# Optimization experiments

Measured on AMD Instinct MI355X. Metric: run time of the kernel, lower is better.

## Reference

```python
import jax, jax.numpy as jnp
from jax import lax
import numpy as np

B, S, G = 64, 200, 8
CHAR_V, GAZ_V = 8000, 100000
D_CHAR, D_GAZ, H = 128, 128, 512
N_LABEL = 20
N_TAG = N_LABEL + 2  # CRF adds START (N_TAG-2) and STOP (N_TAG-1)


def setup_inputs() -> dict:
    key = jax.random.key(0)
    ks = jax.random.split(key, 16)
    lengths = jax.random.randint(ks[0], (B,), S // 2, S + 1)
    pos = jnp.arange(S)[None, :]
    mask = pos < lengths[:, None]
    char_inputs = jax.random.randint(ks[1], (B, S), 0, CHAR_V)
    gaz_ids = jax.random.randint(ks[2], (B, S, G), 0, GAZ_V)
    cnt = jax.random.randint(ks[3], (B, S), 1, G + 1)
    gaz_mask = (jnp.arange(G)[None, None, :] < cnt[..., None]).astype(jnp.int32)
    rev_gaz_ids = jax.random.randint(ks[4], (B, S, G), 0, GAZ_V)
    rcnt = jax.random.randint(ks[5], (B, S), 1, G + 1)
    rev_gaz_mask = (jnp.arange(G)[None, None, :] < rcnt[..., None]).astype(jnp.int32)
    sc = 0.1
    D_in = D_CHAR + D_GAZ
    return dict(
        char_inputs=char_inputs, lengths=lengths, mask=mask,
        gaz_ids=gaz_ids, gaz_mask=gaz_mask,
        rev_gaz_ids=rev_gaz_ids, rev_gaz_mask=rev_gaz_mask,
        char_table=jax.random.normal(ks[6], (CHAR_V, D_CHAR)) * sc,
        gaz_table=jax.random.normal(ks[7], (GAZ_V, D_GAZ)) * sc,
        w_ih_f=jax.random.normal(ks[8], (4 * H, D_in)) * sc,
        w_hh_f=jax.random.normal(ks[9], (4 * H, H)) * sc,
        b_f=jnp.zeros((4 * H,), jnp.float32),
        w_ih_b=jax.random.normal(ks[10], (4 * H, D_in)) * sc,
        w_hh_b=jax.random.normal(ks[11], (4 * H, H)) * sc,
        b_b=jnp.zeros((4 * H,), jnp.float32),
        W_out=jax.random.normal(ks[12], (2 * H, N_TAG)) * sc,
        b_out=jnp.zeros((N_TAG,), jnp.float32),
        transitions=jax.random.normal(ks[13], (N_TAG, N_TAG)) * sc,
    )


def rev_pad(x, lengths):
    # reverse each sequence within its valid length (reverse_padded_sequence)
    b, s = x.shape[0], x.shape[1]
    pos = jnp.arange(s)[None, :]
    idx = jnp.where(pos < lengths[:, None], lengths[:, None] - 1 - pos, pos)
    idx = idx.reshape((b, s) + (1,) * (x.ndim - 2))
    return jnp.take_along_axis(x, jnp.broadcast_to(idx, x.shape), axis=1)


def gaz_embed(table, ids, m):
    # masked mean over the G candidate gaz words per char (Gaz_Embed, type=1)
    e = table[ids]                                   # [B,S,G,D]
    mf = m.astype(e.dtype)[..., None]
    return (e * mf).sum(2) / jnp.maximum(mf.sum(2), 1.0)


def lstm(x, w_ih, w_hh, b):
    # x: [B,S,D]; torch gate order i,f,g,o
    h0 = jnp.zeros((x.shape[0], H), x.dtype)

    def step(carry, xt):
        h, c = carry
        g = xt @ w_ih.T + h @ w_hh.T + b
        i, f, gg, o = jnp.split(g, 4, axis=-1)
        c = jax.nn.sigmoid(f) * c + jax.nn.sigmoid(i) * jnp.tanh(gg)
        h = jax.nn.sigmoid(o) * jnp.tanh(c)
        return (h, c), h

    _, hs = lax.scan(step, (h0, h0), x.transpose(1, 0, 2))
    return hs.transpose(1, 0, 2)                     # [B,S,H]


def emissions_fn(char_inputs, lengths, gaz_ids, gaz_mask, rev_gaz_ids, rev_gaz_mask,
                 char_table, gaz_table, w_ih_f, w_hh_f, b_f, w_ih_b, w_hh_b, b_b,
                 W_out, b_out):
    char_embs = char_table[char_inputs]              # [B,S,Dc]
    rev_char_embs = rev_pad(char_embs, lengths)
    g_f = gaz_embed(gaz_table, gaz_ids, gaz_mask)
    g_b = gaz_embed(gaz_table, rev_pad(rev_gaz_ids, lengths), rev_pad(rev_gaz_mask, lengths))
    fwd_in = jnp.concatenate([char_embs, g_f], axis=-1)
    bwd_in = jnp.concatenate([rev_char_embs, g_b], axis=-1)
    h_f = lstm(fwd_in, w_ih_f, w_hh_f, b_f)
    h_b = rev_pad(lstm(bwd_in, w_ih_b, w_hh_b, b_b), lengths)
    lstm_outs = jnp.concatenate([h_f, h_b], axis=-1)  # [B,S,2H]
    return lstm_outs @ W_out + b_out                  # [B,S,N_TAG]


def viterbi(emissions, mask, transitions):
    # transitions[prev, next]; START=N_TAG-2, STOP=N_TAG-1
    n = emissions.shape[-1]
    start, stop = n - 2, n - 1
    init = emissions[:, 0] + transitions[start][None, :]     # [B,n]
    ident = jnp.arange(n, dtype=jnp.int32)[None, :]

    def vstep(part, inp):
        emit_t, m_t = inp                                    # [B,n], [B]
        cand = part[:, :, None] + transitions[None] + emit_t[:, None, :]
        new = cand.max(axis=1)
        bp = cand.argmax(axis=1).astype(jnp.int32)
        part = jnp.where(m_t[:, None], new, part)
        bp = jnp.where(m_t[:, None], bp, ident)              # identity bp on pad
        return part, bp

    part, bps = lax.scan(vstep, init,
                         (emissions[:, 1:].transpose(1, 0, 2), mask[:, 1:].T))
    last_tag = (part + transitions[:, stop][None, :]).argmax(-1).astype(jnp.int32)

    def btstep(tag, bp):
        prev = jnp.take_along_axis(bp, tag[:, None], axis=1)[:, 0]
        return prev, prev

    _, prev_tags = lax.scan(btstep, last_tag, bps, reverse=True)  # [S-1,B]
    tags = jnp.concatenate([prev_tags.T, last_tag[:, None]], axis=1)
    return tags * mask.astype(tags.dtype)


def reference(char_inputs, lengths, mask, gaz_ids, gaz_mask, rev_gaz_ids, rev_gaz_mask,
              char_table, gaz_table, w_ih_f, w_hh_f, b_f, w_ih_b, w_hh_b, b_b,
              W_out, b_out, transitions):
    emissions = emissions_fn(char_inputs, lengths, gaz_ids, gaz_mask,
                             rev_gaz_ids, rev_gaz_mask, char_table, gaz_table,
                             w_ih_f, w_hh_f, b_f, w_ih_b, w_hh_b, b_b, W_out, b_out)
    return viterbi(emissions, mask, transitions)
```

## Files before the change

### kernel.cpp

```cpp
#include <hip/hip_runtime.h>
#include <math.h>

#define S_LEN 200
#define BATCH 64
#define HID   512
#define NTAG  22
#define TCH   25
#define MC    (TCH*BATCH)

typedef unsigned short u16;
typedef unsigned int   u32;

__device__ __forceinline__ float bf2f(u16 u){
  union { u32 ui; float f; } v; v.ui = ((u32)u) << 16; return v.f;
}

__global__ void k_detect(const u32* __restrict__ w, int* __restrict__ flag){
  __shared__ int cnt;
  if (threadIdx.x == 0) cnt = 0;
  __syncthreads();
  int hits = 0;
  for (int i = threadIdx.x; i < 16384; i += 256){
    u32 e = (w[i] & 0x7F80u);
    if (e >= 0x3800u && e <= 0x4080u) hits++;
  }
  atomicAdd(&cnt, hits);
  __syncthreads();
  if (threadIdx.x == 0) *flag = (cnt > 8192) ? 1 : 0;
}

__global__ void k_cvt_f(const void* __restrict__ src, float* __restrict__ dst,
                        int n, const int* __restrict__ flag){
  int i = blockIdx.x*blockDim.x + threadIdx.x;
  if (i >= n) return;
  if (*flag) dst[i] = bf2f(((const u16*)src)[i]);
  else       dst[i] = ((const float*)src)[i];
}

__global__ void k_cvt_wt(const void* __restrict__ src, float* __restrict__ dst,
                         const int* __restrict__ flag){
  int i = blockIdx.x*blockDim.x + threadIdx.x;
  if (i >= 1024*24) return;
  int k = i / 24, tag = i % 24;
  float v = 0.f;
  if (tag < NTAG){
    v = (*flag) ? bf2f(((const u16*)src)[k*NTAG + tag])
                : ((const float*)src)[k*NTAG + tag];
  }
  int half = k >> 9, kk = k & 511;
  dst[((size_t)half*512 + kk)*24 + tag] = v;
}

__global__ void k_zero(float* __restrict__ p, int n){
  int i = blockIdx.x*blockDim.x + threadIdx.x;
  if (i < n) p[i] = 0.f;
}

__global__ __launch_bounds__(128)
void k_build(const int* __restrict__ ci, const int* __restrict__ lengths,
             const int* __restrict__ gid, const int* __restrict__ gm,
             const int* __restrict__ rgid, const int* __restrict__ rgm,
             const void* __restrict__ ctab, const void* __restrict__ gtab,
             const int* __restrict__ flag,
             float* __restrict__ fin, float* __restrict__ bin)
{
  int bs = blockIdx.x;
  int b = bs / S_LEN, s = bs % S_LEN;
  int d = threadIdx.x;
  int isbf = *flag;
  int len = lengths[b];
  int sb = (s < len) ? (len - 1 - s) : s;
  size_t orow = ((size_t)s*BATCH + b)*256;

  {
    int cid = ci[bs];
    float cv = isbf ? bf2f(((const u16*)ctab)[(size_t)cid*128 + d])
                    : ((const float*)ctab)[(size_t)cid*128 + d];
    fin[orow + d] = cv;
    const int* gg = gid + (size_t)bs*8;
    const int* mm = gm  + (size_t)bs*8;
    float sum = 0.f, cntf = 0.f;
    for (int g = 0; g < 8; ++g){
      float m = (float)mm[g];
      int gw = gg[g];
      float gv = isbf ? bf2f(((const u16*)gtab)[(size_t)gw*128 + d])
                      : ((const float*)gtab)[(size_t)gw*128 + d];
      sum += m * gv; cntf += m;
    }
    fin[orow + 128 + d] = sum / fmaxf(cntf, 1.f);
  }
  {
    int bsr = b*S_LEN + sb;
    int cid = ci[bsr];
    float cv = isbf ? bf2f(((const u16*)ctab)[(size_t)cid*128 + d])
                    : ((const float*)ctab)[(size_t)cid*128 + d];
    bin[orow + d] = cv;
    const int* gg = rgid + (size_t)bsr*8;
    const int* mm = rgm  + (size_t)bsr*8;
    float sum = 0.f, cntf = 0.f;
    for (int g = 0; g < 8; ++g){
      float m = (float)mm[g];
      int gw = gg[g];
      float gv = isbf ? bf2f(((const u16*)gtab)[(size_t)gw*128 + d])
                      : ((const float*)gtab)[(size_t)gw*128 + d];
      sum += m * gv; cntf += m;
    }
    bin[orow + 128 + d] = sum / fmaxf(cntf, 1.f);
  }
}

__global__ __launch_bounds__(256)
void k_gemm_ih(const float* __restrict__ Af, const float* __restrict__ Ab,
               const float* __restrict__ wih,
               const float* __restrict__ bias,
               float* __restrict__ gxc,
               int t0)
{
  const int dir = blockIdx.z;
  const float* A = (dir ? Ab : Af) + (size_t)t0*BATCH*256;
  const float* W = wih + (size_t)dir*2048*256;
  const float* bi = bias + (size_t)dir*2048;
  float* C = gxc + (size_t)dir*2048*MC;
  const int m0 = blockIdx.y * 64;
  const int n0 = blockIdx.x * 64;
  const int tid = threadIdx.x;
  __shared__ float As[32][64];
  __shared__ float Ws[32][64];
  const int lr = tid >> 2;
  const int kq = (tid & 3) * 8;
  const int tx = tid & 15;
  const int ty = tid >> 4;
  float acc[4][4] = {};

  for (int k0 = 0; k0 < 256; k0 += 32){
    float4 a0 = *(const float4*)(A + (size_t)(m0+lr)*256 + k0 + kq);
    float4 a1 = *(const float4*)(A + (size_t)(m0+lr)*256 + k0 + kq + 4);
    float4 w0 = *(const float4*)(W + (size_t)(n0+lr)*256 + k0 + kq);
    float4 w1 = *(const float4*)(W + (size_t)(n0+lr)*256 + k0 + kq + 4);
    As[kq+0][lr]=a0.x; As[kq+1][lr]=a0.y; As[kq+2][lr]=a0.z; As[kq+3][lr]=a0.w;
    As[kq+4][lr]=a1.x; As[kq+5][lr]=a1.y; As[kq+6][lr]=a1.z; As[kq+7][lr]=a1.w;
    Ws[kq+0][lr]=w0.x; Ws[kq+1][lr]=w0.y; Ws[kq+2][lr]=w0.z; Ws[kq+3][lr]=w0.w;
    Ws[kq+4][lr]=w1.x; Ws[kq+5][lr]=w1.y; Ws[kq+6][lr]=w1.z; Ws[kq+7][lr]=w1.w;
    __syncthreads();
    #pragma unroll 8
    for (int kk = 0; kk < 32; ++kk){
      float4 av = *(const float4*)(&As[kk][ty*4]);
      float4 wv = *(const float4*)(&Ws[kk][tx*4]);
      acc[0][0]+=av.x*wv.x; acc[0][1]+=av.x*wv.y; acc[0][2]+=av.x*wv.z; acc[0][3]+=av.x*wv.w;
      acc[1][0]+=av.y*wv.x; acc[1][1]+=av.y*wv.y; acc[1][2]+=av.y*wv.z; acc[1][3]+=av.y*wv.w;
      acc[2][0]+=av.z*wv.x; acc[2][1]+=av.z*wv.y; acc[2][2]+=av.z*wv.z; acc[2][3]+=av.z*wv.w;
      acc[3][0]+=av.w*wv.x; acc[3][1]+=av.w*wv.y; acc[3][2]+=av.w*wv.z; acc[3][3]+=av.w*wv.w;
    }
    __syncthreads();
  }

  #pragma unroll
  for (int j = 0; j < 4; ++j){
    float bj = bi[n0 + tx*4 + j];
    float4 o = make_float4(acc[0][j]+bj, acc[1][j]+bj, acc[2][j]+bj, acc[3][j]+bj);
    *(float4*)(C + (size_t)(n0 + tx*4 + j)*MC + m0 + ty*4) = o;
  }
}

__global__ __launch_bounds__(512)
void k_step(const float* __restrict__ whh,
            const float* __restrict__ gxc,
            float* __restrict__ hbuf,
            float* __restrict__ cbuf,
            float* __restrict__ hseq,
            int t, int tc)
{
  const int dir = blockIdx.y;
  const int hrow_base = blockIdx.x * 4;
  const int tid = threadIdx.x;
  const int b = tid & 63;
  const int uw = __builtin_amdgcn_readfirstlane(tid >> 6);
  const int uk0 = uw * 64;

  __shared__ float part[8*16*64];

  const float* hprev = hbuf + (size_t)(dir*2 + (t&1))*HID*BATCH;
  float* hnext       = hbuf + (size_t)(dir*2 + ((t+1)&1))*HID*BATCH;
  const float* whhd  = whh + (size_t)dir*2048*512;

  float hv[64];
  #pragma unroll
  for (int j = 0; j < 64; ++j)
    hv[j] = hprev[(size_t)(uk0 + j)*BATCH + b];

  float acc[16];
  #pragma unroll
  for (int r = 0; r < 16; ++r) acc[r] = 0.f;

  #pragma unroll
  for (int r = 0; r < 16; ++r){
    const int row_glob = (r >> 2)*512 + hrow_base + (r & 3);
    const float* wr = whhd + (size_t)row_glob*512 + uk0;
    #pragma unroll
    for (int j = 0; j < 64; ++j)
      acc[r] += wr[j] * hv[j];
  }

  #pragma unroll
  for (int r = 0; r < 16; ++r)
    part[(uw*16 + r)*64 + b] = acc[r];
  __syncthreads();

  if (tid < 256){
    const int hr = tid >> 6;
    const int bb = tid & 63;
    const int hrow = hrow_base + hr;
    float g4[4];
    #pragma unroll
    for (int g = 0; g < 4; ++g){
      const int r = g*4 + hr;
      float s = 0.f;
      #pragma unroll
      for (int ww = 0; ww < 8; ++ww)
        s += part[(ww*16 + r)*64 + bb];
      g4[g] = s;
    }
    const float* gxb = gxc + (size_t)dir*2048*MC + (size_t)tc*BATCH + bb;
    float gi = g4[0] + gxb[(size_t)(   0 + hrow)*MC];
    float gf = g4[1] + gxb[(size_t)( 512 + hrow)*MC];
    float gg = g4[2] + gxb[(size_t)(1024 + hrow)*MC];
    float go = g4[3] + gxb[(size_t)(1536 + hrow)*MC];
    float si = 1.f/(1.f+expf(-gi));
    float sf = 1.f/(1.f+expf(-gf));
    float so = 1.f/(1.f+expf(-go));
    size_t ci_ = ((size_t)dir*HID + hrow)*BATCH + bb;
    float c = cbuf[ci_];
    c = sf*c + si*tanhf(gg);
    float h = so*tanhf(c);
    cbuf[ci_] = c;
    hnext[(size_t)hrow*BATCH + bb] = h;
    hseq[(((size_t)dir*S_LEN + t)*HID + hrow)*BATCH + bb] = h;
  }
}

__global__ __launch_bounds__(256)
void k_emis(const float* __restrict__ hseq, const int* __restrict__ lengths,
            const float* __restrict__ wpad,
            const float* __restrict__ bout,
            float* __restrict__ emisF, float* __restrict__ emisB)
{
  const int t = blockIdx.x;
  const int dir = blockIdx.y;
  const int tid = threadIdx.x;
  const int b = tid & 63;
  const int utg = __builtin_amdgcn_readfirstlane(tid >> 6);

  __shared__ float hl[64*64];

  const float* hsrc = hseq + ((size_t)(dir*S_LEN + t)*HID)*BATCH;
  const float* wbase = wpad + (size_t)dir*512*24 + utg*6;

  float acc[6] = {0.f,0.f,0.f,0.f,0.f,0.f};

  for (int c = 0; c < 8; ++c){
    const float4* s4 = (const float4*)(hsrc + (size_t)c*64*64);
    float4* d4 = (float4*)hl;
    #pragma unroll
    for (int q = 0; q < 4; ++q) d4[q*256 + tid] = s4[q*256 + tid];
    __syncthreads();
    const float* wrow = wbase + (size_t)c*64*24;
    #pragma unroll 4
    for (int k = 0; k < 64; ++k){
      float hval = hl[k*64 + b];
      #pragma unroll
      for (int i = 0; i < 6; ++i) acc[i] += hval * wrow[k*24 + i];
    }
    __syncthreads();
  }

  const int len = lengths[b];
  const int pos = dir ? ((t < len) ? (len - 1 - t) : t) : t;
  float* dst = (dir ? emisB : emisF) + ((size_t)b*S_LEN + pos)*NTAG;
  #pragma unroll
  for (int i = 0; i < 6; ++i){
    int tag = utg*6 + i;
    if (tag < NTAG) dst[tag] = acc[i] + (dir ? 0.f : bout[tag]);
  }
}

__global__ __launch_bounds__(64)
void k_viterbi(const float* __restrict__ emisF, const float* __restrict__ emisB,
               const int* __restrict__ lengths,
               const float* __restrict__ trans, int* __restrict__ out)
{
  int b = blockIdx.x;
  int j = threadIdx.x;
  __shared__ float tr[NTAG*NTAG];
  __shared__ float part[NTAG];
  __shared__ unsigned char bp[(S_LEN-1)*NTAG];
  for (int i = j; i < NTAG*NTAG; i += 64) tr[i] = trans[i];
  int len = lengths[b];
  const float* ef = emisF + (size_t)b*S_LEN*NTAG;
  const float* eb = emisB + (size_t)b*S_LEN*NTAG;
  __syncthreads();
  if (j < NTAG) part[j] = ef[j] + eb[j] + tr[(NTAG-2)*NTAG + j];
  __syncthreads();
  for (int t = 1; t < S_LEN; ++t){
    float best = -3.4e38f; int bi = 0;
    if (j < NTAG){
      float e = ef[t*NTAG + j] + eb[t*NTAG + j];
      for (int i = 0; i < NTAG; ++i){
        float v = part[i] + tr[i*NTAG + j] + e;
        if (v > best){ best = v; bi = i; }
      }
    }
    __syncthreads();
    if (j < NTAG){
      if (t < len){ part[j] = best; bp[(t-1)*NTAG + j] = (unsigned char)bi; }
      else        { bp[(t-1)*NTAG + j] = (unsigned char)j; }
    }
    __syncthreads();
  }
  if (j == 0){
    float best = -3.4e38f; int tag = 0;
    for (int i = 0; i < NTAG; ++i){
      float v = part[i] + tr[i*NTAG + (NTAG-1)];
      if (v > best){ best = v; tag = i; }
    }
    out[b*S_LEN + S_LEN-1] = (S_LEN-1 < len) ? tag : 0;
    for (int t = S_LEN-2; t >= 0; --t){
      tag = bp[t*NTAG + tag];
      out[b*S_LEN + t] = (t < len) ? tag : 0;
    }
  }
}

extern "C" void kernel_launch(void* const* d_in, const int* in_sizes, int n_in,
                              void* d_out, int out_size, void* d_ws, size_t ws_size,
                              hipStream_t stream)
{
  (void)in_sizes; (void)n_in; (void)out_size; (void)ws_size;
  const int* char_inputs  = (const int*)d_in[0];
  const int* lengths      = (const int*)d_in[1];
  const int* gaz_ids      = (const int*)d_in[3];
  const int* gaz_mask     = (const int*)d_in[4];
  const int* rev_gaz_ids  = (const int*)d_in[5];
  const int* rev_gaz_mask = (const int*)d_in[6];
  const void* char_table  = d_in[7];
  const void* gaz_table   = d_in[8];
  const void* w_ih_f = d_in[9];
  const void* w_hh_f = d_in[10];
  const void* b_f    = d_in[11];
  const void* w_ih_b = d_in[12];
  const void* w_hh_b = d_in[13];
  const void* b_b    = d_in[14];
  const void* W_out  = d_in[15];
  const void* b_out  = d_in[16];
  const void* trans  = d_in[17];

  char* ws = (char*)d_ws;
  size_t off = 0;
  auto alloc = [&](size_t bytes)->char*{
    char* p = ws + off; off = (off + bytes + 255) & ~(size_t)255; return p;
  };
  int*   flag   = (int*)  alloc(256);
  float* whh32  = (float*)alloc(2ull*2048*512*4);
  float* wih32  = (float*)alloc(2ull*2048*256*4);
  float* bias32 = (float*)alloc(2ull*2048*4);
  float* wpad   = (float*)alloc(2ull*512*24*4);
  float* bout32 = (float*)alloc(22ull*4);
  float* trans32= (float*)alloc(484ull*4);
  float* fwd_in = (float*)alloc(12800ull*256*4);
  float* bwd_in = (float*)alloc(12800ull*256*4);
  float* gxc    = (float*)alloc(2ull*2048*MC*4);
  float* hbuf   = (float*)alloc(2ull*2*512*64*4);
  float* cbuf   = (float*)alloc(2ull*512*64*4);
  float* hseq   = (float*)alloc(2ull*200*512*64*4);
  float* emisF  = (float*)alloc(12800ull*22*4);
  float* emisB  = (float*)alloc(12800ull*22*4);

  k_detect<<<1,256,0,stream>>>((const u32*)char_table, flag);
  k_cvt_f<<<4096,256,0,stream>>>(w_hh_f, whh32,           1048576, flag);
  k_cvt_f<<<4096,256,0,stream>>>(w_hh_b, whh32 + 1048576, 1048576, flag);
  k_cvt_f<<<2048,256,0,stream>>>(w_ih_f, wih32,            524288, flag);
  k_cvt_f<<<2048,256,0,stream>>>(w_ih_b, wih32 + 524288,   524288, flag);
  k_cvt_f<<<8,256,0,stream>>>(b_f, bias32,        2048, flag);
  k_cvt_f<<<8,256,0,stream>>>(b_b, bias32 + 2048, 2048, flag);
  k_cvt_wt<<<96,256,0,stream>>>(W_out, wpad, flag);
  k_cvt_f<<<1,256,0,stream>>>(b_out, bout32, 22, flag);
  k_cvt_f<<<2,256,0,stream>>>(trans, trans32, 484, flag);

  k_build<<<12800,128,0,stream>>>(char_inputs, lengths, gaz_ids, gaz_mask,
                                  rev_gaz_ids, rev_gaz_mask, char_table, gaz_table,
                                  flag, fwd_in, bwd_in);

  k_zero<<<768,256,0,stream>>>(hbuf, 2*2*512*64 + 2*512*64);

  for (int t0 = 0; t0 < S_LEN; t0 += TCH){
    k_gemm_ih<<<dim3(32,TCH,2),256,0,stream>>>(fwd_in, bwd_in, wih32, bias32,
                                               gxc, t0);
    for (int tc = 0; tc < TCH; ++tc)
      k_step<<<dim3(128,2),512,0,stream>>>(whh32, gxc, hbuf, cbuf, hseq, t0+tc, tc);
  }

  k_emis<<<dim3(S_LEN,2),256,0,stream>>>(hseq, lengths, wpad, bout32, emisF, emisB);
  k_viterbi<<<64,64,0,stream>>>(emisF, emisB, lengths, trans32, (int*)d_out);
}
```

Before: 2.812 ms.

## Swizzle recurrent weights, widen input GEMM tile, shuffle-based Viterbi, fuse small conversions

Recurrent weights are pre-permuted into a per-block, per-wave contiguous layout, so each k_step block reads its slice linearly instead of striding across four gate row groups. The LSTM step also issues its gate-input and cell-state loads before the matvec so their latency overlaps it. The input-projection GEMM moves to 64x128 tiles with 8x4 accumulators per thread. Viterbi now keeps state in registers and uses wave shuffles instead of shared memory and block barriers. Several small conversion launches are merged into one to cut launch overhead.

```diff
diff --git a/kernel.cpp b/kernel.cpp
--- a/kernel.cpp
+++ b/kernel.cpp
@@ -35,6 +35,32 @@
   if (i >= n) return;
   if (*flag) dst[i] = bf2f(((const u16*)src)[i]);
   else       dst[i] = ((const float*)src)[i];
+}
+
+__global__ void k_cvt4(const void* s0, float* d0, int n0,
+                       const void* s1, float* d1, int n1,
+                       const void* s2, float* d2, int n2,
+                       const void* s3, float* d3, int n3,
+                       const int* __restrict__ flag){
+  int i = blockIdx.x*blockDim.x + threadIdx.x;
+  int isbf = *flag;
+  if (i < n0) d0[i] = isbf ? bf2f(((const u16*)s0)[i]) : ((const float*)s0)[i];
+  if (i < n1) d1[i] = isbf ? bf2f(((const u16*)s1)[i]) : ((const float*)s1)[i];
+  if (i < n2) d2[i] = isbf ? bf2f(((const u16*)s2)[i]) : ((const float*)s2)[i];
+  if (i < n3) d3[i] = isbf ? bf2f(((const u16*)s3)[i]) : ((const float*)s3)[i];
+}
+
+__global__ __launch_bounds__(256)
+void k_cvt_whh(const void* __restrict__ wf, const void* __restrict__ wb,
+               float* __restrict__ dst, const int* __restrict__ flag){
+  int o = blockIdx.x*256 + threadIdx.x;
+  if (o >= 2*2048*512) return;
+  int j = o & 63, r = (o>>6)&15, w = (o>>10)&7, slice = (o>>13)&127, dir = o>>20;
+  int row = (r>>2)*512 + slice*4 + (r&3);
+  int si = row*512 + w*64 + j;
+  const void* src = dir ? wb : wf;
+  float v = (*flag) ? bf2f(((const u16*)src)[si]) : ((const float*)src)[si];
+  dst[o] = v;
 }
 
 __global__ void k_cvt_wt(const void* __restrict__ src, float* __restrict__ dst,
@@ -122,48 +148,59 @@
   const float* bi = bias + (size_t)dir*2048;
   float* C = gxc + (size_t)dir*2048*MC;
   const int m0 = blockIdx.y * 64;
-  const int n0 = blockIdx.x * 64;
+  const int n0 = blockIdx.x * 128;
   const int tid = threadIdx.x;
   __shared__ float As[32][64];
-  __shared__ float Ws[32][64];
-  const int lr = tid >> 2;
-  const int kq = (tid & 3) * 8;
-  const int tx = tid & 15;
-  const int ty = tid >> 4;
-  float acc[4][4] = {};
+  __shared__ float Ws[32][128];
+  const int lrA = tid >> 2, kqA = (tid & 3)*8;
+  const int lrW = tid >> 1, kqW = (tid & 1)*16;
+  const int tx = tid & 31, ty = tid >> 5;
+  float acc[8][4] = {};
 
   for (int k0 = 0; k0 < 256; k0 += 32){
-    float4 a0 = *(const float4*)(A + (size_t)(m0+lr)*256 + k0 + kq);
-    float4 a1 = *(const float4*)(A + (size_t)(m0+lr)*256 + k0 + kq + 4);
-    float4 w0 = *(const float4*)(W + (size_t)(n0+lr)*256 + k0 + kq);
-    float4 w1 = *(const float4*)(W + (size_t)(n0+lr)*256 + k0 + kq + 4);
-    As[kq+0][lr]=a0.x; As[kq+1][lr]=a0.y; As[kq+2][lr]=a0.z; As[kq+3][lr]=a0.w;
-    As[kq+4][lr]=a1.x; As[kq+5][lr]=a1.y; As[kq+6][lr]=a1.z; As[kq+7][lr]=a1.w;
-    Ws[kq+0][lr]=w0.x; Ws[kq+1][lr]=w0.y; Ws[kq+2][lr]=w0.z; Ws[kq+3][lr]=w0.w;
-    Ws[kq+4][lr]=w1.x; Ws[kq+5][lr]=w1.y; Ws[kq+6][lr]=w1.z; Ws[kq+7][lr]=w1.w;
+    float4 a0 = *(const float4*)(A + (size_t)(m0+lrA)*256 + k0+kqA);
+    float4 a1 = *(const float4*)(A + (size_t)(m0+lrA)*256 + k0+kqA+4);
+    float4 w0 = *(const float4*)(W + (size_t)(n0+lrW)*256 + k0+kqW);
+    float4 w1 = *(const float4*)(W + (size_t)(n0+lrW)*256 + k0+kqW+4);
+    float4 w2 = *(const float4*)(W + (size_t)(n0+lrW)*256 + k0+kqW+8);
+    float4 w3 = *(const float4*)(W + (size_t)(n0+lrW)*256 + k0+kqW+12);
+    As[kqA+0][lrA]=a0.x; As[kqA+1][lrA]=a0.y; As[kqA+2][lrA]=a0.z; As[kqA+3][lrA]=a0.w;
+    As[kqA+4][lrA]=a1.x; As[kqA+5][lrA]=a1.y; As[kqA+6][lrA]=a1.z; As[kqA+7][lrA]=a1.w;
+    Ws[kqW+ 0][lrW]=w0.x; Ws[kqW+ 1][lrW]=w0.y; Ws[kqW+ 2][lrW]=w0.z; Ws[kqW+ 3][lrW]=w0.w;
+    Ws[kqW+ 4][lrW]=w1.x; Ws[kqW+ 5][lrW]=w1.y; Ws[kqW+ 6][lrW]=w1.z; Ws[kqW+ 7][lrW]=w1.w;
+    Ws[kqW+ 8][lrW]=w2.x; Ws[kqW+ 9][lrW]=w2.y; Ws[kqW+10][lrW]=w2.z; Ws[kqW+11][lrW]=w2.w;
+    Ws[kqW+12][lrW]=w3.x; Ws[kqW+13][lrW]=w3.y; Ws[kqW+14][lrW]=w3.z; Ws[kqW+15][lrW]=w3.w;
     __syncthreads();
     #pragma unroll 8
     for (int kk = 0; kk < 32; ++kk){
-      float4 av = *(const float4*)(&As[kk][ty*4]);
-      float4 wv = *(const float4*)(&Ws[kk][tx*4]);
-      acc[0][0]+=av.x*wv.x; acc[0][1]+=av.x*wv.y; acc[0][2]+=av.x*wv.z; acc[0][3]+=av.x*wv.w;
-      acc[1][0]+=av.y*wv.x; acc[1][1]+=av.y*wv.y; acc[1][2]+=av.y*wv.z; acc[1][3]+=av.y*wv.w;
-      acc[2][0]+=av.z*wv.x; acc[2][1]+=av.z*wv.y; acc[2][2]+=av.z*wv.z; acc[2][3]+=av.z*wv.w;
-      acc[3][0]+=av.w*wv.x; acc[3][1]+=av.w*wv.y; acc[3][2]+=av.w*wv.z; acc[3][3]+=av.w*wv.w;
+      float4 av0 = *(const float4*)(&As[kk][ty*8]);
+      float4 av1 = *(const float4*)(&As[kk][ty*8+4]);
+      float4 wv  = *(const float4*)(&Ws[kk][tx*4]);
+      acc[0][0]+=av0.x*wv.x; acc[0][1]+=av0.x*wv.y; acc[0][2]+=av0.x*wv.z; acc[0][3]+=av0.x*wv.w;
+      acc[1][0]+=av0.y*wv.x; acc[1][1]+=av0.y*wv.y; acc[1][2]+=av0.y*wv.z; acc[1][3]+=av0.y*wv.w;
+      acc[2][0]+=av0.z*wv.x; acc[2][1]+=av0.z*wv.y; acc[2][2]+=av0.z*wv.z; acc[2][3]+=av0.z*wv.w;
+      acc[3][0]+=av0.w*wv.x; acc[3][1]+=av0.w*wv.y; acc[3][2]+=av0.w*wv.z; acc[3][3]+=av0.w*wv.w;
+      acc[4][0]+=av1.x*wv.x; acc[4][1]+=av1.x*wv.y; acc[4][2]+=av1.x*wv.z; acc[4][3]+=av1.x*wv.w;
+      acc[5][0]+=av1.y*wv.x; acc[5][1]+=av1.y*wv.y; acc[5][2]+=av1.y*wv.z; acc[5][3]+=av1.y*wv.w;
+      acc[6][0]+=av1.z*wv.x; acc[6][1]+=av1.z*wv.y; acc[6][2]+=av1.z*wv.z; acc[6][3]+=av1.z*wv.w;
+      acc[7][0]+=av1.w*wv.x; acc[7][1]+=av1.w*wv.y; acc[7][2]+=av1.w*wv.z; acc[7][3]+=av1.w*wv.w;
     }
     __syncthreads();
   }
 
   #pragma unroll
-  for (int j = 0; j < 4; ++j){
-    float bj = bi[n0 + tx*4 + j];
-    float4 o = make_float4(acc[0][j]+bj, acc[1][j]+bj, acc[2][j]+bj, acc[3][j]+bj);
-    *(float4*)(C + (size_t)(n0 + tx*4 + j)*MC + m0 + ty*4) = o;
+  for (int jn = 0; jn < 4; ++jn){
+    int col = n0 + tx*4 + jn;
+    float bj = bi[col];
+    float4 o0 = make_float4(acc[0][jn]+bj, acc[1][jn]+bj, acc[2][jn]+bj, acc[3][jn]+bj);
+    float4 o1 = make_float4(acc[4][jn]+bj, acc[5][jn]+bj, acc[6][jn]+bj, acc[7][jn]+bj);
+    *(float4*)(C + (size_t)col*MC + m0 + ty*8)     = o0;
+    *(float4*)(C + (size_t)col*MC + m0 + ty*8 + 4) = o1;
   }
 }
 
 __global__ __launch_bounds__(512)
-void k_step(const float* __restrict__ whh,
+void k_step(const float* __restrict__ wsw,
             const float* __restrict__ gxc,
             float* __restrict__ hbuf,
             float* __restrict__ cbuf,
@@ -171,7 +208,8 @@
             int t, int tc)
 {
   const int dir = blockIdx.y;
-  const int hrow_base = blockIdx.x * 4;
+  const int slice = blockIdx.x;
+  const int hrow_base = slice*4;
   const int tid = threadIdx.x;
   const int b = tid & 63;
   const int uw = __builtin_amdgcn_readfirstlane(tid >> 6);
@@ -181,21 +219,33 @@
 
   const float* hprev = hbuf + (size_t)(dir*2 + (t&1))*HID*BATCH;
   float* hnext       = hbuf + (size_t)(dir*2 + ((t+1)&1))*HID*BATCH;
-  const float* whhd  = whh + (size_t)dir*2048*512;
+
+  float pgi=0.f, pgf=0.f, pgg=0.f, pgo=0.f, pc=0.f;
+  if (tid < 256){
+    const int hr = tid >> 6, bb = tid & 63;
+    const int hrow = hrow_base + hr;
+    const float* gxb = gxc + (size_t)dir*2048*MC + (size_t)tc*BATCH + bb;
+    pgi = gxb[(size_t)(   0 + hrow)*MC];
+    pgf = gxb[(size_t)( 512 + hrow)*MC];
+    pgg = gxb[(size_t)(1024 + hrow)*MC];
+    pgo = gxb[(size_t)(1536 + hrow)*MC];
+    pc  = cbuf[((size_t)dir*HID + hrow)*BATCH + bb];
+  }
 
   float hv[64];
   #pragma unroll
   for (int j = 0; j < 64; ++j)
     hv[j] = hprev[(size_t)(uk0 + j)*BATCH + b];
 
+  const float* wv_base = wsw + (((size_t)(dir*128 + slice))*8 + uw)*1024;
+
   float acc[16];
   #pragma unroll
   for (int r = 0; r < 16; ++r) acc[r] = 0.f;
 
   #pragma unroll
   for (int r = 0; r < 16; ++r){
-    const int row_glob = (r >> 2)*512 + hrow_base + (r & 3);
-    const float* wr = whhd + (size_t)row_glob*512 + uk0;
+    const float* wr = wv_base + r*64;
     #pragma unroll
     for (int j = 0; j < 64; ++j)
       acc[r] += wr[j] * hv[j];
@@ -220,19 +270,16 @@
         s += part[(ww*16 + r)*64 + bb];
       g4[g] = s;
     }
-    const float* gxb = gxc + (size_t)dir*2048*MC + (size_t)tc*BATCH + bb;
-    float gi = g4[0] + gxb[(size_t)(   0 + hrow)*MC];
-    float gf = g4[1] + gxb[(size_t)( 512 + hrow)*MC];
-    float gg = g4[2] + gxb[(size_t)(1024 + hrow)*MC];
-    float go = g4[3] + gxb[(size_t)(1536 + hrow)*MC];
+    float gi = g4[0] + pgi;
+    float gf = g4[1] + pgf;
+    float gg = g4[2] + pgg;
+    float go = g4[3] + pgo;
     float si = 1.f/(1.f+expf(-gi));
     float sf = 1.f/(1.f+expf(-gf));
     float so = 1.f/(1.f+expf(-go));
-    size_t ci_ = ((size_t)dir*HID + hrow)*BATCH + bb;
-    float c = cbuf[ci_];
-    c = sf*c + si*tanhf(gg);
+    float c = sf*pc + si*tanhf(gg);
     float h = so*tanhf(c);
-    cbuf[ci_] = c;
+    cbuf[((size_t)dir*HID + hrow)*BATCH + bb] = c;
     hnext[(size_t)hrow*BATCH + bb] = h;
     hseq[(((size_t)dir*S_LEN + t)*HID + hrow)*BATCH + bb] = h;
   }
@@ -288,40 +335,45 @@
                const int* __restrict__ lengths,
                const float* __restrict__ trans, int* __restrict__ out)
 {
-  int b = blockIdx.x;
-  int j = threadIdx.x;
-  __shared__ float tr[NTAG*NTAG];
-  __shared__ float part[NTAG];
+  const int b = blockIdx.x;
+  const int j = threadIdx.x;
   __shared__ unsigned char bp[(S_LEN-1)*NTAG];
-  for (int i = j; i < NTAG*NTAG; i += 64) tr[i] = trans[i];
-  int len = lengths[b];
+  const int len = lengths[b];
   const float* ef = emisF + (size_t)b*S_LEN*NTAG;
   const float* eb = emisB + (size_t)b*S_LEN*NTAG;
-  __syncthreads();
-  if (j < NTAG) part[j] = ef[j] + eb[j] + tr[(NTAG-2)*NTAG + j];
-  __syncthreads();
+  const bool act = (j < NTAG);
+
+  float trc[NTAG];
+  #pragma unroll
+  for (int i = 0; i < NTAG; ++i)
+    trc[i] = act ? trans[i*NTAG + j] : 0.f;
+  const float trstop = act ? trans[j*NTAG + (NTAG-1)] : 0.f;
+
+  float part = act ? (ef[j] + eb[j] + trans[(NTAG-2)*NTAG + j]) : -3.4e38f;
+  float e_next = act ? (ef[NTAG + j] + eb[NTAG + j]) : 0.f;
+
   for (int t = 1; t < S_LEN; ++t){
+    float e = e_next;
+    if (t+1 < S_LEN && act) e_next = ef[(t+1)*NTAG + j] + eb[(t+1)*NTAG + j];
     float best = -3.4e38f; int bi = 0;
-    if (j < NTAG){
-      float e = ef[t*NTAG + j] + eb[t*NTAG + j];
-      for (int i = 0; i < NTAG; ++i){
-        float v = part[i] + tr[i*NTAG + j] + e;
-        if (v > best){ best = v; bi = i; }
-      }
-    }
-    __syncthreads();
-    if (j < NTAG){
-      if (t < len){ part[j] = best; bp[(t-1)*NTAG + j] = (unsigned char)bi; }
-      else        { bp[(t-1)*NTAG + j] = (unsigned char)j; }
-    }
-    __syncthreads();
-  }
+    #pragma unroll
+    for (int i = 0; i < NTAG; ++i){
+      float v = __shfl(part, i) + trc[i];
+      if (v > best){ best = v; bi = i; }
+    }
+    if (t < len) part = best + e;
+    if (act) bp[(t-1)*NTAG + j] = (unsigned char)((t < len) ? bi : j);
+  }
+
+  float fin = part + trstop;
+  float best = -3.4e38f; int tag = 0;
+  #pragma unroll
+  for (int i = 0; i < NTAG; ++i){
+    float v = __shfl(fin, i);
+    if (v > best){ best = v; tag = i; }
+  }
+  __builtin_amdgcn_wave_barrier();
   if (j == 0){
-    float best = -3.4e38f; int tag = 0;
-    for (int i = 0; i < NTAG; ++i){
-      float v = part[i] + tr[i*NTAG + (NTAG-1)];
-      if (v > best){ best = v; tag = i; }
-    }
     out[b*S_LEN + S_LEN-1] = (S_LEN-1 < len) ? tag : 0;
     for (int t = S_LEN-2; t >= 0; --t){
       tag = bp[t*NTAG + tag];
@@ -359,7 +411,7 @@
     char* p = ws + off; off = (off + bytes + 255) & ~(size_t)255; return p;
   };
   int*   flag   = (int*)  alloc(256);
-  float* whh32  = (float*)alloc(2ull*2048*512*4);
+  float* wsw    = (float*)alloc(2ull*2048*512*4);
   float* wih32  = (float*)alloc(2ull*2048*256*4);
   float* bias32 = (float*)alloc(2ull*2048*4);
   float* wpad   = (float*)alloc(2ull*512*24*4);
@@ -375,15 +427,14 @@
   float* emisB  = (float*)alloc(12800ull*22*4);
 
   k_detect<<<1,256,0,stream>>>((const u32*)char_table, flag);
-  k_cvt_f<<<4096,256,0,stream>>>(w_hh_f, whh32,           1048576, flag);
-  k_cvt_f<<<4096,256,0,stream>>>(w_hh_b, whh32 + 1048576, 1048576, flag);
-  k_cvt_f<<<2048,256,0,stream>>>(w_ih_f, wih32,            524288, flag);
-  k_cvt_f<<<2048,256,0,stream>>>(w_ih_b, wih32 + 524288,   524288, flag);
-  k_cvt_f<<<8,256,0,stream>>>(b_f, bias32,        2048, flag);
-  k_cvt_f<<<8,256,0,stream>>>(b_b, bias32 + 2048, 2048, flag);
+  k_cvt_whh<<<8192,256,0,stream>>>(w_hh_f, w_hh_b, wsw, flag);
+  k_cvt_f<<<2048,256,0,stream>>>(w_ih_f, wih32,          524288, flag);
+  k_cvt_f<<<2048,256,0,stream>>>(w_ih_b, wih32 + 524288, 524288, flag);
+  k_cvt4<<<8,256,0,stream>>>(b_f, bias32, 2048,
+                             b_b, bias32 + 2048, 2048,
+                             b_out, bout32, 22,
+                             trans, trans32, 484, flag);
   k_cvt_wt<<<96,256,0,stream>>>(W_out, wpad, flag);
-  k_cvt_f<<<1,256,0,stream>>>(b_out, bout32, 22, flag);
-  k_cvt_f<<<2,256,0,stream>>>(trans, trans32, 484, flag);
 
   k_build<<<12800,128,0,stream>>>(char_inputs, lengths, gaz_ids, gaz_mask,
                                   rev_gaz_ids, rev_gaz_mask, char_table, gaz_table,
@@ -392,10 +443,10 @@
   k_zero<<<768,256,0,stream>>>(hbuf, 2*2*512*64 + 2*512*64);
 
   for (int t0 = 0; t0 < S_LEN; t0 += TCH){
-    k_gemm_ih<<<dim3(32,TCH,2),256,0,stream>>>(fwd_in, bwd_in, wih32, bias32,
+    k_gemm_ih<<<dim3(16,TCH,2),256,0,stream>>>(fwd_in, bwd_in, wih32, bias32,
                                                gxc, t0);
     for (int tc = 0; tc < TCH; ++tc)
-      k_step<<<dim3(128,2),512,0,stream>>>(whh32, gxc, hbuf, cbuf, hseq, t0+tc, tc);
+      k_step<<<dim3(128,2),512,0,stream>>>(wsw, gxc, hbuf, cbuf, hseq, t0+tc, tc);
   }
 
   k_emis<<<dim3(S_LEN,2),256,0,stream>>>(hseq, lengths, wpad, bout32, emisF, emisB);
```

Result: slower. 2.886 ms (+2.6%).
